# Performance work log

Measured on AMD Instinct MI355X. Metric: run time of the kernel, lower is better.

The kernel has to match this reference:

```python
import jax, jax.numpy as jnp
import numpy as np
from jax import lax

EPS = 1e-5

def layernorm_c(x, w, b):
    # WithBias LayerNorm over channel dim per spatial location (Restormer style)
    mu = jnp.mean(x, axis=1, keepdims=True)
    var = jnp.var(x, axis=1, keepdims=True)  # population variance (unbiased=False)
    xn = (x - mu) / jnp.sqrt(var + EPS)
    return xn * w[None, :, None, None] + b[None, :, None, None]

def conv1x1(x, w, b):
    # w: (C_out, C_in)
    y = jnp.einsum('bchw,oc->bohw', x, w)
    return y + b[None, :, None, None]

def dwconv3x3(x, w, b):
    # w: (C, 1, 3, 3), depthwise
    y = lax.conv_general_dilated(x, w, window_strides=(1, 1), padding=((1, 1), (1, 1)),
                                 dimension_numbers=('NCHW', 'OIHW', 'NCHW'),
                                 feature_group_count=x.shape[1])
    return y + b[None, :, None, None]

def to_patches(x, p):
    B, C, H, W = x.shape
    x = x.reshape(B, C, H // p, p, W // p, p)
    return x.transpose(0, 1, 2, 4, 3, 5)  # (B,C,h,w,p,p)

def from_patches(x):
    B, C, h, w, p1, p2 = x.shape
    return x.transpose(0, 1, 2, 4, 3, 5).reshape(B, C, h * p1, w * p2)

def setup_inputs() -> dict:
    key = jax.random.key(0)
    ks = jax.random.split(key, 12)
    B, C, H, W = 8, 128, 192, 192
    s = 0.05
    return {
        'x': jax.random.normal(ks[0], (B, C, H, W), jnp.float32),
        'evt': jax.random.normal(ks[1], (B, C, H, W), jnp.float32),
        'ln_img_w': jnp.ones((C,), jnp.float32),
        'ln_img_b': jnp.zeros((C,), jnp.float32),
        'ln_evt_w': jnp.ones((C,), jnp.float32),
        'ln_evt_b': jnp.zeros((C,), jnp.float32),
        'q_w': jax.random.normal(ks[2], (2 * C, C), jnp.float32) * s,
        'q_b': jnp.zeros((2 * C,), jnp.float32),
        'q_dw_w': jax.random.normal(ks[3], (2 * C, 1, 3, 3), jnp.float32) * s,
        'q_dw_b': jnp.zeros((2 * C,), jnp.float32),
        'kv_w': jax.random.normal(ks[4], (4 * C, C), jnp.float32) * s,
        'kv_b': jnp.zeros((4 * C,), jnp.float32),
        'kv_dw_w': jax.random.normal(ks[5], (4 * C, 1, 3, 3), jnp.float32) * s,
        'kv_dw_b': jnp.zeros((4 * C,), jnp.float32),
        'ln_corr_w': jnp.ones((2 * C,), jnp.float32),
        'ln_corr_b': jnp.zeros((2 * C,), jnp.float32),
        'proj_w': jax.random.normal(ks[6], (C, 2 * C), jnp.float32) * s,
        'proj_b': jnp.zeros((C,), jnp.float32),
    }

def reference(x, evt, ln_img_w, ln_img_b, ln_evt_w, ln_evt_b,
              q_w, q_b, q_dw_w, q_dw_b, kv_w, kv_b, kv_dw_w, kv_dw_b,
              ln_corr_w, ln_corr_b, proj_w, proj_b):
    p = 8
    C = x.shape[1]
    xn = layernorm_c(x, ln_img_w, ln_img_b)
    en = layernorm_c(evt, ln_evt_w, ln_evt_b)
    q = dwconv3x3(conv1x1(xn, q_w, q_b), q_dw_w, q_dw_b)          # (B,2C,H,W)
    kv = dwconv3x3(conv1x1(en, kv_w, kv_b), kv_dw_w, kv_dw_b)      # (B,4C,H,W)
    k, v = kv[:, :2 * C], kv[:, 2 * C:]
    q_p = to_patches(q, p)  # (B,2C,h,w,p,p)
    k_p = to_patches(k, p)
    corr = jnp.fft.irfft2(jnp.fft.rfft2(q_p.astype(jnp.float32)) *
                          jnp.fft.rfft2(k_p.astype(jnp.float32)), s=(p, p))
    corr = from_patches(corr)                                      # (B,2C,H,W)
    corr = layernorm_c(corr, ln_corr_w, ln_corr_b)
    return conv1x1(v * corr, proj_w, proj_b)
```

## Files before the change

kernel.cpp:

```cpp
#include <hip/hip_runtime.h>
#include <stdint.h>

#define BATCH 8
#define CIN   128
#define HH    192
#define WW    192
#define HW    (HH*WW)
#define PXB   576
#define CH    2
#define RS    216

typedef _Float16 half_t;
typedef _Float16 f16x8 __attribute__((ext_vector_type(8)));
typedef _Float16 f16x4 __attribute__((ext_vector_type(4)));
typedef _Float16 f16x2 __attribute__((ext_vector_type(2)));
typedef float    f32x4 __attribute__((ext_vector_type(4)));
typedef float    f32x16 __attribute__((ext_vector_type(16)));
typedef unsigned int u32;

__device__ __forceinline__ float DOT2(u32 a, u32 b, float c) {
#if __has_builtin(__builtin_amdgcn_fdot2)
    return __builtin_amdgcn_fdot2(__builtin_bit_cast(f16x2, a),
                                  __builtin_bit_cast(f16x2, b), c, false);
#else
    f16x2 av = __builtin_bit_cast(f16x2, a), bv = __builtin_bit_cast(f16x2, b);
    return c + (float)av[0] * (float)bv[0] + (float)av[1] * (float)bv[1];
#endif
}

#define SMEM_BYTES 52736
#define WSH_OFF    17408
#define MU_OFF     52224

__global__ __launch_bounds__(256)
void wcvt_kernel(const float* __restrict__ qw, const float* __restrict__ kvw,
                 const float* __restrict__ pw, const float* __restrict__ qdw,
                 const float* __restrict__ kvdw, half_t* __restrict__ out)
{
    int q = blockIdx.x * 256 + threadIdx.x;
    if (q >= 34496) return;
    int idx = q * 4;
    const float* src;
    int off;
    if (idx < 32768)       { src = qw;   off = idx; }
    else if (idx < 98304)  { src = kvw;  off = idx - 32768; }
    else if (idx < 131072) { src = pw;   off = idx - 98304; }
    else if (idx < 133376) { src = qdw;  off = idx - 131072; }
    else                   { src = kvdw; off = idx - 133376; }
    float4 v = *(const float4*)&src[off];
    f16x4 o = { (half_t)v.x, (half_t)v.y, (half_t)v.z, (half_t)v.w };
    *(f16x4*)&out[idx] = o;
}

template<int OC>
__global__ __launch_bounds__(256)
void ln_gemm_kernel(const float* __restrict__ x,
                    const float* __restrict__ lnw, const float* __restrict__ lnb,
                    const half_t* __restrict__ wf16, const float* __restrict__ wb,
                    half_t* __restrict__ out)
{
    __shared__ __attribute__((aligned(16))) char smem[SMEM_BYTES];
    half_t (*As)[136]  = (half_t(*)[136])smem;
    half_t (*Wsh)[136] = (half_t(*)[136])(smem + WSH_OFF);
    float  (*Cst)[68]  = (float (*)[68]) (smem + WSH_OFF);
    float* redA = (float*)(smem + WSH_OFF);
    float* redB = (float*)(smem + WSH_OFF + 1024);
    float* mu_s = (float*)(smem + MU_OFF);
    float* rs_s = mu_s + 64;

    const int tid  = threadIdx.x;
    const int px   = tid & 63;
    const int g    = tid >> 6;
    const int l    = tid & 63;
    const int w    = tid >> 6;
    const int lrow = l & 31;
    const int lk   = (l >> 5) * 8;

    const long p0  = (long)blockIdx.x * 64;
    const int  b   = (int)(p0 / HW);
    const int  hw0 = (int)(p0 - (long)b * HW);

    const float* xb = x + (size_t)b * CIN * HW + hw0 + px;
    float vals[32];
    float s1 = 0.f, s2 = 0.f;
#pragma unroll
    for (int j = 0; j < 32; ++j) {
        float v = xb[(size_t)(g * 32 + j) * HW];
        vals[j] = v; s1 += v; s2 += v * v;
    }
    redA[g * 64 + px] = s1; redB[g * 64 + px] = s2;
    __syncthreads();
    if (tid < 64) {
        float su = redA[tid] + redA[64 + tid] + redA[128 + tid] + redA[192 + tid];
        float sq = redB[tid] + redB[64 + tid] + redB[128 + tid] + redB[192 + tid];
        float mu  = su * (1.f / 128.f);
        float var = sq * (1.f / 128.f) - mu * mu;
        mu_s[tid] = mu;
        rs_s[tid] = rsqrtf(var + 1e-5f);
    }
    __syncthreads();
    {
        float mu = mu_s[px], rs = rs_s[px];
#pragma unroll
        for (int m = 0; m < 4; ++m) {
            f16x8 o;
#pragma unroll
            for (int j = 0; j < 8; ++j) {
                int c = g * 32 + m * 8 + j;
                o[j] = (half_t)((vals[m * 8 + j] - mu) * rs * lnw[c] + lnb[c]);
            }
            *(f16x8*)&As[px][g * 32 + m * 8] = o;
        }
    }

    for (int nc = 0; nc < OC / 128; ++nc) {
        const int n0 = nc * 128;
        if (nc) __syncthreads();
#pragma unroll
        for (int i = 0; i < 8; ++i) {
            int f  = i * 256 + tid;
            int n  = f >> 4;
            int xh = (f & 15) * 8;
            *(f16x8*)&Wsh[n][xh] = *(const f16x8*)&wf16[(size_t)(n0 + n) * CIN + xh];
        }
        __syncthreads();

        f16x8 af[8];
#pragma unroll
        for (int kk = 0; kk < 8; ++kk)
            af[kk] = *(const f16x8*)&Wsh[w * 32 + lrow][kk * 16 + lk];

        f32x16 acc0, acc1;
#pragma unroll
        for (int i = 0; i < 16; ++i) { acc0[i] = 0.f; acc1[i] = 0.f; }
#pragma unroll
        for (int kk = 0; kk < 8; ++kk) {
            f16x8 b0 = *(const f16x8*)&As[lrow][kk * 16 + lk];
            f16x8 b1 = *(const f16x8*)&As[32 + lrow][kk * 16 + lk];
            acc0 = __builtin_amdgcn_mfma_f32_32x32x16_f16(af[kk], b0, acc0, 0, 0, 0);
            acc1 = __builtin_amdgcn_mfma_f32_32x32x16_f16(af[kk], b1, acc1, 0, 0, 0);
        }
        __syncthreads();

#pragma unroll
        for (int r = 0; r < 16; ++r) {
            int oc = w * 32 + (r & 3) + 8 * (r >> 2) + 4 * (l >> 5);
            Cst[oc][lrow]      = acc0[r];
            Cst[oc][32 + lrow] = acc1[r];
        }
        __syncthreads();

#pragma unroll
        for (int i = 0; i < 4; ++i) {
            int idx = i * 256 + tid;
            int oc  = idx >> 3;
            int pxg = idx & 7;
            const float4 a = *(const float4*)&Cst[oc][pxg * 8];
            const float4 c = *(const float4*)&Cst[oc][pxg * 8 + 4];
            float bias = wb[n0 + oc];
            f16x8 o = { (half_t)(a.x + bias), (half_t)(a.y + bias),
                        (half_t)(a.z + bias), (half_t)(a.w + bias),
                        (half_t)(c.x + bias), (half_t)(c.y + bias),
                        (half_t)(c.z + bias), (half_t)(c.w + bias) };
            *(f16x8*)&out[((size_t)b * OC + n0 + oc) * HW + hw0 + pxg * 8] = o;
        }
    }
}

__global__ __launch_bounds__(256)
void corr_strip_kernel(const half_t* __restrict__ q1, const half_t* __restrict__ kv1,
                       const half_t* __restrict__ qdw16, const float* __restrict__ qb,
                       const half_t* __restrict__ kdw16, const float* __restrict__ kb,
                       half_t* __restrict__ corr, half_t* __restrict__ vd)
{
    __shared__ __attribute__((aligned(16))) half_t raw[6][10][RS];
    __shared__ __attribute__((aligned(16))) half_t qd[2][8][RS];
    __shared__ __attribute__((aligned(16))) half_t krev[2][8][RS];

    const int bid = blockIdx.x;
    const int cg  = bid & 127;
    const int ph  = (bid >> 7) % 24;
    const int lb  = (bid >> 7) / 24;
    const int c0  = cg * CH;
    const int tid = threadIdx.x;

    if (tid < 120) {
        int side = tid & 1;
        int row  = (tid >> 1) % 10;
        int a    = tid / 20;
        f16x8 z = {};
        *(f16x8*)&raw[a][row][side ? 200 : 0] = z;
    }

    for (int i = 0; i < 6; ++i) {
        int idx = tid + 256 * i;
        if (idx >= 1440) break;
        int vec = idx % 24;
        int row = (idx / 24) % 10;
        int a   = idx / 240;
        int ch  = a & 1;
        int gh  = ph * 8 - 1 + row;
        f16x8 v = {};
        if (gh >= 0 && gh < HH) {
            const half_t* src;
            if (a < 2)      src = q1  + ((size_t)lb * 256 + c0 + ch) * HW;
            else if (a < 4) src = kv1 + ((size_t)lb * 512 + c0 + ch) * HW;
            else            src = kv1 + ((size_t)lb * 512 + 256 + c0 + ch) * HW;
            v = *(const f16x8*)&src[(size_t)gh * WW + vec * 8];
        }
        *(f16x8*)&raw[a][row][8 + vec * 8] = v;
    }
    __syncthreads();

    for (int i = 0; i < 3; ++i) {
        int unit = tid + 256 * i;
        if (unit >= 576) break;
        int u   = unit & 7;
        int xg2 = (unit >> 3) % 12;
        int a   = unit / 96;
        int ch  = a & 1;
        const half_t (*rw)[RS] = raw[a];
        const half_t* wt;
        float bias;
        if (a < 2)      { wt = qdw16 + (size_t)(c0 + ch) * 9;       bias = qb[c0 + ch]; }
        else if (a < 4) { wt = kdw16 + (size_t)(c0 + ch) * 9;       bias = kb[c0 + ch]; }
        else            { wt = kdw16 + (size_t)(256 + c0 + ch) * 9; bias = kb[256 + c0 + ch]; }
        u32 w01[3], w2z[3];
#pragma unroll
        for (int dy = 0; dy < 3; ++dy) {
            u32 a0 = (u32)__builtin_bit_cast(unsigned short, wt[dy * 3 + 0]);
            u32 a1 = (u32)__builtin_bit_cast(unsigned short, wt[dy * 3 + 1]);
            u32 a2 = (u32)__builtin_bit_cast(unsigned short, wt[dy * 3 + 2]);
            w01[dy] = a0 | (a1 << 16);
            w2z[dy] = a2;
        }
        const int x0 = xg2 * 16;
        float acc[16];
#pragma unroll
        for (int xx = 0; xx < 16; ++xx) acc[xx] = bias;
#pragma unroll
        for (int dy = 0; dy < 3; ++dy) {
            const half_t* rowp = &rw[u + dy][x0];
            uint4 c0v = *(const uint4*)(rowp);
            uint4 c1v = *(const uint4*)(rowp + 8);
            uint4 c2v = *(const uint4*)(rowp + 16);
            uint4 c3v = *(const uint4*)(rowp + 24);
            u32 H[13] = {c0v.x,c0v.y,c0v.z,c0v.w, c1v.x,c1v.y,c1v.z,c1v.w,
                         c2v.x,c2v.y,c2v.z,c2v.w, c3v.x};
            u32 A[12];
#pragma unroll
            for (int m = 3; m < 12; ++m) A[m] = (H[m] >> 16) | (H[m + 1] << 16);
#pragma unroll
            for (int xx = 0; xx < 16; ++xx) {
                u32 p01 = (xx & 1) ? H[(7 + xx) >> 1] : A[3 + (xx >> 1)];
                u32 p2  = (xx & 1) ? H[(9 + xx) >> 1] : A[4 + (xx >> 1)];
                acc[xx] = DOT2(p01, w01[dy], acc[xx]);
                acc[xx] = DOT2(p2,  w2z[dy], acc[xx]);
            }
        }
        f16x8 o0, o1;
#pragma unroll
        for (int xx = 0; xx < 8; ++xx) { o0[xx] = (half_t)acc[xx]; o1[xx] = (half_t)acc[8 + xx]; }
        if (a < 2) {
            *(f16x8*)&qd[ch][u][x0]     = o0;
            *(f16x8*)&qd[ch][u][x0 + 8] = o1;
        } else if (a < 4) {
            f16x8 r0v, r1v;
            r0v[0] = (half_t)acc[0];
            r1v[0] = (half_t)acc[8];
#pragma unroll
            for (int j = 1; j < 8; ++j) {
                r0v[j] = (half_t)acc[8 - j];
                r1v[j] = (half_t)acc[16 - j];
            }
            *(f16x8*)&krev[ch][u][x0]     = r0v;
            *(f16x8*)&krev[ch][u][x0 + 8] = r1v;
        } else {
            half_t* dst = &vd[((size_t)lb * 256 + c0 + ch) * HW + (size_t)(ph * 8 + u) * WW + x0];
            *(f16x8*)dst       = o0;
            *(f16x8*)(dst + 8) = o1;
        }
    }
    __syncthreads();

    for (int i = 0; i < 2; ++i) {
        int unit = tid + 256 * i;
        if (unit >= 384) break;
        int c   = unit / 192;
        int rem = unit % 192;
        int pw  = rem >> 3;
        int u   = rem & 7;
        float acc[8];
#pragma unroll
        for (int v = 0; v < 8; ++v) acc[v] = 0.f;
#pragma unroll
        for (int s = 0; s < 8; ++s) {
            int r = (u - s) & 7;
            uint4 q4 = *(const uint4*)&qd[c][s][pw * 8];
            uint4 k4 = *(const uint4*)&krev[c][r][pw * 8];
            u32 Q[4] = {q4.x, q4.y, q4.z, q4.w};
            u32 K[4] = {k4.x, k4.y, k4.z, k4.w};
            u32 S[4];
#pragma unroll
            for (int m = 0; m < 4; ++m) S[m] = (K[m] >> 16) | (K[(m + 1) & 3] << 16);
#pragma unroll
            for (int v = 0; v < 8; ++v) {
                const int o = 8 - v;
#pragma unroll
                for (int tt = 0; tt < 4; ++tt) {
                    u32 pr = (o & 1) ? S[(((o - 1) >> 1) + tt) & 3]
                                     : K[((o >> 1) + tt) & 3];
                    acc[v] = DOT2(Q[tt], pr, acc[v]);
                }
            }
        }
        f16x8 ov;
#pragma unroll
        for (int v = 0; v < 8; ++v) ov[v] = (half_t)acc[v];
        *(f16x8*)&corr[((size_t)lb * 256 + c0 + c) * HW + (size_t)(ph * 8 + u) * WW + pw * 8] = ov;
    }
}

__global__ __launch_bounds__(256)
void proj_kernel(const half_t* __restrict__ corr, const half_t* __restrict__ vd,
                 const float* __restrict__ lnw, const float* __restrict__ lnb,
                 const half_t* __restrict__ wp16, const float* __restrict__ wb,
                 float* __restrict__ out)
{
    __shared__ __attribute__((aligned(16))) char smem[SMEM_BYTES];
    half_t (*As)[136]  = (half_t(*)[136])smem;
    half_t (*Wsh)[136] = (half_t(*)[136])(smem + WSH_OFF);
    float  (*Cst)[68]  = (float (*)[68]) (smem + WSH_OFF);
    float* redA = (float*)(smem + WSH_OFF);
    float* redB = (float*)(smem + WSH_OFF + 1024);
    float* mu_s = (float*)(smem + MU_OFF);
    float* rs_s = mu_s + 64;

    const int tid  = threadIdx.x;
    const int px   = tid & 63;
    const int g    = tid >> 6;
    const int l    = tid & 63;
    const int w    = tid >> 6;
    const int lrow = l & 31;
    const int lk   = (l >> 5) * 8;

    const long p0  = (long)blockIdx.x * 64;
    const int  lb  = (int)(p0 / HW);
    const int  hw0 = (int)(p0 - (long)lb * HW);

    const half_t* cb = corr + (size_t)lb * 256 * HW + hw0 + px;
    const half_t* vb = vd   + (size_t)lb * 256 * HW + hw0 + px;

    float s1 = 0.f, s2 = 0.f;
#pragma unroll 8
    for (int j = 0; j < 64; ++j) {
        float cv = (float)cb[(size_t)(g * 64 + j) * HW];
        s1 += cv; s2 += cv * cv;
    }
    redA[g * 64 + px] = s1; redB[g * 64 + px] = s2;
    __syncthreads();
    if (tid < 64) {
        float su = redA[tid] + redA[64 + tid] + redA[128 + tid] + redA[192 + tid];
        float sq = redB[tid] + redB[64 + tid] + redB[128 + tid] + redB[192 + tid];
        float mu  = su * (1.f / 256.f);
        float var = sq * (1.f / 256.f) - mu * mu;
        mu_s[tid] = mu;
        rs_s[tid] = rsqrtf(var + 1e-5f);
    }
    __syncthreads();
    const float mu = mu_s[px], rs = rs_s[px];

    f32x16 acc0, acc1;
#pragma unroll
    for (int i = 0; i < 16; ++i) { acc0[i] = 0.f; acc1[i] = 0.f; }

    for (int kc = 0; kc < 2; ++kc) {
        if (kc) __syncthreads();
#pragma unroll
        for (int m = 0; m < 4; ++m) {
            f16x8 o;
#pragma unroll
            for (int j = 0; j < 8; ++j) {
                int c = kc * 128 + g * 32 + m * 8 + j;
                float cv = (float)cb[(size_t)c * HW];
                float vv = (float)vb[(size_t)c * HW];
                o[j] = (half_t)(((cv - mu) * rs * lnw[c] + lnb[c]) * vv);
            }
            *(f16x8*)&As[px][g * 32 + m * 8] = o;
        }
#pragma unroll
        for (int i = 0; i < 8; ++i) {
            int f  = i * 256 + tid;
            int n  = f >> 4;
            int xh = (f & 15) * 8;
            *(f16x8*)&Wsh[n][xh] = *(const f16x8*)&wp16[(size_t)n * 256 + kc * 128 + xh];
        }
        __syncthreads();

        f16x8 af[8];
#pragma unroll
        for (int kk = 0; kk < 8; ++kk)
            af[kk] = *(const f16x8*)&Wsh[w * 32 + lrow][kk * 16 + lk];
#pragma unroll
        for (int kk = 0; kk < 8; ++kk) {
            f16x8 b0 = *(const f16x8*)&As[lrow][kk * 16 + lk];
            f16x8 b1 = *(const f16x8*)&As[32 + lrow][kk * 16 + lk];
            acc0 = __builtin_amdgcn_mfma_f32_32x32x16_f16(af[kk], b0, acc0, 0, 0, 0);
            acc1 = __builtin_amdgcn_mfma_f32_32x32x16_f16(af[kk], b1, acc1, 0, 0, 0);
        }
    }
    __syncthreads();

#pragma unroll
    for (int r = 0; r < 16; ++r) {
        int oc = w * 32 + (r & 3) + 8 * (r >> 2) + 4 * (l >> 5);
        Cst[oc][lrow]      = acc0[r];
        Cst[oc][32 + lrow] = acc1[r];
    }
    __syncthreads();

#pragma unroll
    for (int i = 0; i < 8; ++i) {
        int idx = i * 256 + tid;
        int oc  = idx >> 4;
        int pxq = idx & 15;
        float4 a = *(const float4*)&Cst[oc][pxq * 4];
        float bias = wb[oc];
        a.x += bias; a.y += bias; a.z += bias; a.w += bias;
        *(float4*)&out[((size_t)lb * 128 + oc) * HW + hw0 + pxq * 4] = a;
    }
}

extern "C" void kernel_launch(void* const* d_in, const int* in_sizes, int n_in,
                              void* d_out, int out_size, void* d_ws, size_t ws_size,
                              hipStream_t stream)
{
    const float* x        = (const float*)d_in[0];
    const float* evt      = (const float*)d_in[1];
    const float* ln_img_w = (const float*)d_in[2];
    const float* ln_img_b = (const float*)d_in[3];
    const float* ln_evt_w = (const float*)d_in[4];
    const float* ln_evt_b = (const float*)d_in[5];
    const float* q_w      = (const float*)d_in[6];
    const float* q_b      = (const float*)d_in[7];
    const float* q_dw_w   = (const float*)d_in[8];
    const float* q_dw_b   = (const float*)d_in[9];
    const float* kv_w     = (const float*)d_in[10];
    const float* kv_b     = (const float*)d_in[11];
    const float* kv_dw_w  = (const float*)d_in[12];
    const float* kv_dw_b  = (const float*)d_in[13];
    const float* ln_corr_w= (const float*)d_in[14];
    const float* ln_corr_b= (const float*)d_in[15];
    const float* proj_w   = (const float*)d_in[16];
    const float* proj_b   = (const float*)d_in[17];
    float* out = (float*)d_out;

    const size_t wtail = (ws_size - 278528) & ~(size_t)255;
    half_t* wf    = (half_t*)((char*)d_ws + wtail);
    half_t* wq16  = wf;
    half_t* wkv16 = wf + 32768;
    half_t* wp16  = wf + 98304;
    half_t* qdw16 = wf + 131072;
    half_t* kdw16 = wf + 133376;

    const size_t per_b = (size_t)(256 + 512 + 256 + 256) * HW * sizeof(half_t);
    int PB = 1;
    if      (wtail >= 8 * per_b) PB = 8;
    else if (wtail >= 4 * per_b) PB = 4;
    else if (wtail >= 2 * per_b) PB = 2;

    half_t* q1   = (half_t*)d_ws;
    half_t* kv1  = q1  + (size_t)PB * 256 * HW;
    half_t* vd   = kv1 + (size_t)PB * 512 * HW;
    half_t* corr = vd  + (size_t)PB * 256 * HW;

    dim3 blk(256);
    wcvt_kernel<<<135, blk, 0, stream>>>(q_w, kv_w, proj_w, q_dw_w, kv_dw_w, wf);

    for (int b0 = 0; b0 < BATCH; b0 += PB) {
        int nb = PB;
        ln_gemm_kernel<256><<<nb * PXB, blk, 0, stream>>>(
            x + (size_t)b0 * CIN * HW, ln_img_w, ln_img_b, wq16, q_b, q1);
        ln_gemm_kernel<512><<<nb * PXB, blk, 0, stream>>>(
            evt + (size_t)b0 * CIN * HW, ln_evt_w, ln_evt_b, wkv16, kv_b, kv1);
        corr_strip_kernel<<<nb * 24 * 128, blk, 0, stream>>>(
            q1, kv1, qdw16, q_dw_b, kdw16, kv_dw_b, corr, vd);
        proj_kernel<<<nb * PXB, blk, 0, stream>>>(
            corr, vd, ln_corr_w, ln_corr_b, wp16, proj_b,
            out + (size_t)b0 * 128 * HW);
    }
}
```

Baseline: 697.2 us.

## Process one batch at a time and fuse projection with next batch's LN-GEMM

```diff
diff --git a/kernel.cpp b/kernel.cpp
--- a/kernel.cpp
+++ b/kernel.cpp
@@ -52,14 +52,12 @@
     *(f16x4*)&out[idx] = o;
 }
 
-template<int OC>
-__global__ __launch_bounds__(256)
-void ln_gemm_kernel(const float* __restrict__ x,
-                    const float* __restrict__ lnw, const float* __restrict__ lnb,
-                    const half_t* __restrict__ wf16, const float* __restrict__ wb,
-                    half_t* __restrict__ out)
-{
-    __shared__ __attribute__((aligned(16))) char smem[SMEM_BYTES];
+__device__ void ln_gemm_body(char* smem, int bid, int OC,
+    const float* __restrict__ x,
+    const float* __restrict__ lnw, const float* __restrict__ lnb,
+    const half_t* __restrict__ wf16, const float* __restrict__ wb,
+    half_t* __restrict__ out)
+{
     half_t (*As)[136]  = (half_t(*)[136])smem;
     half_t (*Wsh)[136] = (half_t(*)[136])(smem + WSH_OFF);
     float  (*Cst)[68]  = (float (*)[68]) (smem + WSH_OFF);
@@ -76,11 +74,9 @@
     const int lrow = l & 31;
     const int lk   = (l >> 5) * 8;
 
-    const long p0  = (long)blockIdx.x * 64;
-    const int  b   = (int)(p0 / HW);
-    const int  hw0 = (int)(p0 - (long)b * HW);
-
-    const float* xb = x + (size_t)b * CIN * HW + hw0 + px;
+    const int hw0 = bid * 64;
+
+    const float* xb = x + hw0 + px;
     float vals[32];
     float s1 = 0.f, s2 = 0.f;
 #pragma unroll
@@ -113,7 +109,7 @@
         }
     }
 
-    for (int nc = 0; nc < OC / 128; ++nc) {
+    for (int nc = 0; nc < (OC >> 7); ++nc) {
         const int n0 = nc * 128;
         if (nc) __syncthreads();
 #pragma unroll
@@ -162,9 +158,149 @@
                         (half_t)(a.z + bias), (half_t)(a.w + bias),
                         (half_t)(c.x + bias), (half_t)(c.y + bias),
                         (half_t)(c.z + bias), (half_t)(c.w + bias) };
-            *(f16x8*)&out[((size_t)b * OC + n0 + oc) * HW + hw0 + pxg * 8] = o;
-        }
-    }
+            *(f16x8*)&out[(size_t)(n0 + oc) * HW + hw0 + pxg * 8] = o;
+        }
+    }
+}
+
+__device__ void proj_body(char* smem, int bid,
+    const half_t* __restrict__ corr, const half_t* __restrict__ vd,
+    const float* __restrict__ lnw, const float* __restrict__ lnb,
+    const half_t* __restrict__ wp16, const float* __restrict__ wb,
+    float* __restrict__ out)
+{
+    half_t (*As)[136]  = (half_t(*)[136])smem;
+    half_t (*Wsh)[136] = (half_t(*)[136])(smem + WSH_OFF);
+    float  (*Cst)[68]  = (float (*)[68]) (smem + WSH_OFF);
+    float* redA = (float*)(smem + WSH_OFF);
+    float* redB = (float*)(smem + WSH_OFF + 1024);
+    float* mu_s = (float*)(smem + MU_OFF);
+    float* rs_s = mu_s + 64;
+
+    const int tid  = threadIdx.x;
+    const int px   = tid & 63;
+    const int g    = tid >> 6;
+    const int l    = tid & 63;
+    const int w    = tid >> 6;
+    const int lrow = l & 31;
+    const int lk   = (l >> 5) * 8;
+
+    const int hw0 = bid * 64;
+
+    const half_t* cb = corr + hw0 + px;
+    const half_t* vb = vd   + hw0 + px;
+
+    float s1 = 0.f, s2 = 0.f;
+#pragma unroll 8
+    for (int j = 0; j < 64; ++j) {
+        float cv = (float)cb[(size_t)(g * 64 + j) * HW];
+        s1 += cv; s2 += cv * cv;
+    }
+    redA[g * 64 + px] = s1; redB[g * 64 + px] = s2;
+    __syncthreads();
+    if (tid < 64) {
+        float su = redA[tid] + redA[64 + tid] + redA[128 + tid] + redA[192 + tid];
+        float sq = redB[tid] + redB[64 + tid] + redB[128 + tid] + redB[192 + tid];
+        float mu  = su * (1.f / 256.f);
+        float var = sq * (1.f / 256.f) - mu * mu;
+        mu_s[tid] = mu;
+        rs_s[tid] = rsqrtf(var + 1e-5f);
+    }
+    __syncthreads();
+    const float mu = mu_s[px], rs = rs_s[px];
+
+    f32x16 acc0, acc1;
+#pragma unroll
+    for (int i = 0; i < 16; ++i) { acc0[i] = 0.f; acc1[i] = 0.f; }
+
+    for (int kc = 0; kc < 2; ++kc) {
+        if (kc) __syncthreads();
+#pragma unroll
+        for (int m = 0; m < 4; ++m) {
+            f16x8 o;
+#pragma unroll
+            for (int j = 0; j < 8; ++j) {
+                int c = kc * 128 + g * 32 + m * 8 + j;
+                float cv = (float)cb[(size_t)c * HW];
+                float vv = (float)vb[(size_t)c * HW];
+                o[j] = (half_t)(((cv - mu) * rs * lnw[c] + lnb[c]) * vv);
+            }
+            *(f16x8*)&As[px][g * 32 + m * 8] = o;
+        }
+#pragma unroll
+        for (int i = 0; i < 8; ++i) {
+            int f  = i * 256 + tid;
+            int n  = f >> 4;
+            int xh = (f & 15) * 8;
+            *(f16x8*)&Wsh[n][xh] = *(const f16x8*)&wp16[(size_t)n * 256 + kc * 128 + xh];
+        }
+        __syncthreads();
+
+        f16x8 af[8];
+#pragma unroll
+        for (int kk = 0; kk < 8; ++kk)
+            af[kk] = *(const f16x8*)&Wsh[w * 32 + lrow][kk * 16 + lk];
+#pragma unroll
+        for (int kk = 0; kk < 8; ++kk) {
+            f16x8 b0 = *(const f16x8*)&As[lrow][kk * 16 + lk];
+            f16x8 b1 = *(const f16x8*)&As[32 + lrow][kk * 16 + lk];
+            acc0 = __builtin_amdgcn_mfma_f32_32x32x16_f16(af[kk], b0, acc0, 0, 0, 0);
+            acc1 = __builtin_amdgcn_mfma_f32_32x32x16_f16(af[kk], b1, acc1, 0, 0, 0);
+        }
+    }
+    __syncthreads();
+
+#pragma unroll
+    for (int r = 0; r < 16; ++r) {
+        int oc = w * 32 + (r & 3) + 8 * (r >> 2) + 4 * (l >> 5);
+        Cst[oc][lrow]      = acc0[r];
+        Cst[oc][32 + lrow] = acc1[r];
+    }
+    __syncthreads();
+
+#pragma unroll
+    for (int i = 0; i < 8; ++i) {
+        int idx = i * 256 + tid;
+        int oc  = idx >> 4;
+        int pxq = idx & 15;
+        float4 a = *(const float4*)&Cst[oc][pxq * 4];
+        float bias = wb[oc];
+        a.x += bias; a.y += bias; a.z += bias; a.w += bias;
+        *(float4*)&out[(size_t)oc * HW + hw0 + pxq * 4] = a;
+    }
+}
+
+__global__ __launch_bounds__(256)
+void ln_pair_kernel(const float* __restrict__ x, const float* __restrict__ evt,
+                    const float* __restrict__ liw, const float* __restrict__ lib,
+                    const float* __restrict__ lew, const float* __restrict__ leb,
+                    const half_t* __restrict__ wq, const float* __restrict__ qb,
+                    const half_t* __restrict__ wkv, const float* __restrict__ kvb,
+                    half_t* __restrict__ q1, half_t* __restrict__ kv1)
+{
+    __shared__ __attribute__((aligned(16))) char smem[SMEM_BYTES];
+    int bid = blockIdx.x;
+    if (bid < PXB) ln_gemm_body(smem, bid, 256, x, liw, lib, wq, qb, q1);
+    else           ln_gemm_body(smem, bid - PXB, 512, evt, lew, leb, wkv, kvb, kv1);
+}
+
+__global__ __launch_bounds__(256)
+void proj_ln_kernel(const half_t* __restrict__ corr, const half_t* __restrict__ vd,
+                    const float* __restrict__ lcw, const float* __restrict__ lcb,
+                    const half_t* __restrict__ wp, const float* __restrict__ pb,
+                    float* __restrict__ out,
+                    const float* __restrict__ x, const float* __restrict__ evt,
+                    const float* __restrict__ liw, const float* __restrict__ lib,
+                    const float* __restrict__ lew, const float* __restrict__ leb,
+                    const half_t* __restrict__ wq, const float* __restrict__ qb,
+                    const half_t* __restrict__ wkv, const float* __restrict__ kvb,
+                    half_t* __restrict__ q1, half_t* __restrict__ kv1)
+{
+    __shared__ __attribute__((aligned(16))) char smem[SMEM_BYTES];
+    int bid = blockIdx.x;
+    if (bid < PXB)          proj_body(smem, bid, corr, vd, lcw, lcb, wp, pb, out);
+    else if (bid < 2 * PXB) ln_gemm_body(smem, bid - PXB, 256, x, liw, lib, wq, qb, q1);
+    else                    ln_gemm_body(smem, bid - 2 * PXB, 512, evt, lew, leb, wkv, kvb, kv1);
 }
 
 __global__ __launch_bounds__(256)
@@ -180,7 +316,6 @@
     const int bid = blockIdx.x;
     const int cg  = bid & 127;
     const int ph  = (bid >> 7) % 24;
-    const int lb  = (bid >> 7) / 24;
     const int c0  = cg * CH;
     const int tid = threadIdx.x;
 
@@ -203,9 +338,9 @@
         f16x8 v = {};
         if (gh >= 0 && gh < HH) {
             const half_t* src;
-            if (a < 2)      src = q1  + ((size_t)lb * 256 + c0 + ch) * HW;
-            else if (a < 4) src = kv1 + ((size_t)lb * 512 + c0 + ch) * HW;
-            else            src = kv1 + ((size_t)lb * 512 + 256 + c0 + ch) * HW;
+            if (a < 2)      src = q1  + (size_t)(c0 + ch) * HW;
+            else if (a < 4) src = kv1 + (size_t)(c0 + ch) * HW;
+            else            src = kv1 + (size_t)(256 + c0 + ch) * HW;
             v = *(const f16x8*)&src[(size_t)gh * WW + vec * 8];
         }
         *(f16x8*)&raw[a][row][8 + vec * 8] = v;
@@ -276,7 +411,7 @@
             *(f16x8*)&krev[ch][u][x0]     = r0v;
             *(f16x8*)&krev[ch][u][x0 + 8] = r1v;
         } else {
-            half_t* dst = &vd[((size_t)lb * 256 + c0 + ch) * HW + (size_t)(ph * 8 + u) * WW + x0];
+            half_t* dst = &vd[(size_t)(c0 + ch) * HW + (size_t)(ph * 8 + u) * WW + x0];
             *(f16x8*)dst       = o0;
             *(f16x8*)(dst + 8) = o1;
         }
@@ -317,117 +452,7 @@
         f16x8 ov;
 #pragma unroll
         for (int v = 0; v < 8; ++v) ov[v] = (half_t)acc[v];
-        *(f16x8*)&corr[((size_t)lb * 256 + c0 + c) * HW + (size_t)(ph * 8 + u) * WW + pw * 8] = ov;
-    }
-}
-
-__global__ __launch_bounds__(256)
-void proj_kernel(const half_t* __restrict__ corr, const half_t* __restrict__ vd,
-                 const float* __restrict__ lnw, const float* __restrict__ lnb,
-                 const half_t* __restrict__ wp16, const float* __restrict__ wb,
-                 float* __restrict__ out)
-{
-    __shared__ __attribute__((aligned(16))) char smem[SMEM_BYTES];
-    half_t (*As)[136]  = (half_t(*)[136])smem;
-    half_t (*Wsh)[136] = (half_t(*)[136])(smem + WSH_OFF);
-    float  (*Cst)[68]  = (float (*)[68]) (smem + WSH_OFF);
-    float* redA = (float*)(smem + WSH_OFF);
-    float* redB = (float*)(smem + WSH_OFF + 1024);
-    float* mu_s = (float*)(smem + MU_OFF);
-    float* rs_s = mu_s + 64;
-
-    const int tid  = threadIdx.x;
-    const int px   = tid & 63;
-    const int g    = tid >> 6;
-    const int l    = tid & 63;
-    const int w    = tid >> 6;
-    const int lrow = l & 31;
-    const int lk   = (l >> 5) * 8;
-
-    const long p0  = (long)blockIdx.x * 64;
-    const int  lb  = (int)(p0 / HW);
-    const int  hw0 = (int)(p0 - (long)lb * HW);
-
-    const half_t* cb = corr + (size_t)lb * 256 * HW + hw0 + px;
-    const half_t* vb = vd   + (size_t)lb * 256 * HW + hw0 + px;
-
-    float s1 = 0.f, s2 = 0.f;
-#pragma unroll 8
-    for (int j = 0; j < 64; ++j) {
-        float cv = (float)cb[(size_t)(g * 64 + j) * HW];
-        s1 += cv; s2 += cv * cv;
-    }
-    redA[g * 64 + px] = s1; redB[g * 64 + px] = s2;
-    __syncthreads();
-    if (tid < 64) {
-        float su = redA[tid] + redA[64 + tid] + redA[128 + tid] + redA[192 + tid];
-        float sq = redB[tid] + redB[64 + tid] + redB[128 + tid] + redB[192 + tid];
-        float mu  = su * (1.f / 256.f);
-        float var = sq * (1.f / 256.f) - mu * mu;
-        mu_s[tid] = mu;
-        rs_s[tid] = rsqrtf(var + 1e-5f);
-    }
-    __syncthreads();
-    const float mu = mu_s[px], rs = rs_s[px];
-
-    f32x16 acc0, acc1;
-#pragma unroll
-    for (int i = 0; i < 16; ++i) { acc0[i] = 0.f; acc1[i] = 0.f; }
-
-    for (int kc = 0; kc < 2; ++kc) {
-        if (kc) __syncthreads();
-#pragma unroll
-        for (int m = 0; m < 4; ++m) {
-            f16x8 o;
-#pragma unroll
-            for (int j = 0; j < 8; ++j) {
-                int c = kc * 128 + g * 32 + m * 8 + j;
-                float cv = (float)cb[(size_t)c * HW];
-                float vv = (float)vb[(size_t)c * HW];
-                o[j] = (half_t)(((cv - mu) * rs * lnw[c] + lnb[c]) * vv);
-            }
-            *(f16x8*)&As[px][g * 32 + m * 8] = o;
-        }
-#pragma unroll
-        for (int i = 0; i < 8; ++i) {
-            int f  = i * 256 + tid;
-            int n  = f >> 4;
-            int xh = (f & 15) * 8;
-            *(f16x8*)&Wsh[n][xh] = *(const f16x8*)&wp16[(size_t)n * 256 + kc * 128 + xh];
-        }
-        __syncthreads();
-
-        f16x8 af[8];
-#pragma unroll
-        for (int kk = 0; kk < 8; ++kk)
-            af[kk] = *(const f16x8*)&Wsh[w * 32 + lrow][kk * 16 + lk];
-#pragma unroll
-        for (int kk = 0; kk < 8; ++kk) {
-            f16x8 b0 = *(const f16x8*)&As[lrow][kk * 16 + lk];
-            f16x8 b1 = *(const f16x8*)&As[32 + lrow][kk * 16 + lk];
-            acc0 = __builtin_amdgcn_mfma_f32_32x32x16_f16(af[kk], b0, acc0, 0, 0, 0);
-            acc1 = __builtin_amdgcn_mfma_f32_32x32x16_f16(af[kk], b1, acc1, 0, 0, 0);
-        }
-    }
-    __syncthreads();
-
-#pragma unroll
-    for (int r = 0; r < 16; ++r) {
-        int oc = w * 32 + (r & 3) + 8 * (r >> 2) + 4 * (l >> 5);
-        Cst[oc][lrow]      = acc0[r];
-        Cst[oc][32 + lrow] = acc1[r];
-    }
-    __syncthreads();
-
-#pragma unroll
-    for (int i = 0; i < 8; ++i) {
-        int idx = i * 256 + tid;
-        int oc  = idx >> 4;
-        int pxq = idx & 15;
-        float4 a = *(const float4*)&Cst[oc][pxq * 4];
-        float bias = wb[oc];
-        a.x += bias; a.y += bias; a.z += bias; a.w += bias;
-        *(float4*)&out[((size_t)lb * 128 + oc) * HW + hw0 + pxq * 4] = a;
+        *(f16x8*)&corr[(size_t)(c0 + c) * HW + (size_t)(ph * 8 + u) * WW + pw * 8] = ov;
     }
 }
 
@@ -463,30 +488,28 @@
     half_t* qdw16 = wf + 131072;
     half_t* kdw16 = wf + 133376;
 
-    const size_t per_b = (size_t)(256 + 512 + 256 + 256) * HW * sizeof(half_t);
-    int PB = 1;
-    if      (wtail >= 8 * per_b) PB = 8;
-    else if (wtail >= 4 * per_b) PB = 4;
-    else if (wtail >= 2 * per_b) PB = 2;
-
     half_t* q1   = (half_t*)d_ws;
-    half_t* kv1  = q1  + (size_t)PB * 256 * HW;
-    half_t* vd   = kv1 + (size_t)PB * 512 * HW;
-    half_t* corr = vd  + (size_t)PB * 256 * HW;
+    half_t* kv1  = q1  + (size_t)256 * HW;
+    half_t* vd   = kv1 + (size_t)512 * HW;
+    half_t* corr = vd  + (size_t)256 * HW;
 
     dim3 blk(256);
     wcvt_kernel<<<135, blk, 0, stream>>>(q_w, kv_w, proj_w, q_dw_w, kv_dw_w, wf);
 
-    for (int b0 = 0; b0 < BATCH; b0 += PB) {
-        int nb = PB;
-        ln_gemm_kernel<256><<<nb * PXB, blk, 0, stream>>>(
-            x + (size_t)b0 * CIN * HW, ln_img_w, ln_img_b, wq16, q_b, q1);
-        ln_gemm_kernel<512><<<nb * PXB, blk, 0, stream>>>(
-            evt + (size_t)b0 * CIN * HW, ln_evt_w, ln_evt_b, wkv16, kv_b, kv1);
-        corr_strip_kernel<<<nb * 24 * 128, blk, 0, stream>>>(
+    ln_pair_kernel<<<2 * PXB, blk, 0, stream>>>(
+        x, evt, ln_img_w, ln_img_b, ln_evt_w, ln_evt_b,
+        wq16, q_b, wkv16, kv_b, q1, kv1);
+
+    for (int i = 0; i < BATCH; ++i) {
+        corr_strip_kernel<<<24 * 128, blk, 0, stream>>>(
             q1, kv1, qdw16, q_dw_b, kdw16, kv_dw_b, corr, vd);
-        proj_kernel<<<nb * PXB, blk, 0, stream>>>(
+        int bn = (i + 1 < BATCH) ? (i + 1) : (BATCH - 1);
+        int grid = (i + 1 < BATCH) ? 3 * PXB : PXB;
+        proj_ln_kernel<<<grid, blk, 0, stream>>>(
             corr, vd, ln_corr_w, ln_corr_b, wp16, proj_b,
-            out + (size_t)b0 * 128 * HW);
-    }
-}
+            out + (size_t)i * 128 * HW,
+            x + (size_t)bn * CIN * HW, evt + (size_t)bn * CIN * HW,
+            ln_img_w, ln_img_b, ln_evt_w, ln_evt_b,
+            wq16, q_b, wkv16, kv_b, q1, kv1);
+    }
+}
```

Measured after the change: 881.7 us. +26.5%, slower.
